# Performance work log

Hardware: AMD Instinct MI355X
Metric: run time of the kernel (lower is better)

## Reference

```python
import jax, jax.numpy as jnp
import numpy as np

GDEP = 2
ALPHA = 0.05

def setup_inputs() -> dict:
    key = jax.random.key(0)
    ks = jax.random.split(key, 6)
    B, C, V, L = 8, 32, 512, 256  # L = c_in * num_patterns
    x = jax.random.normal(ks[0], (B, C, V, L), dtype=jnp.float32)
    adj = jax.random.uniform(ks[1], (B, V, V), dtype=jnp.float32)
    W = jax.random.normal(ks[2], (L, L), dtype=jnp.float32) * (1.0 / np.sqrt(L))
    b = jax.random.normal(ks[3], (L,), dtype=jnp.float32) * (1.0 / np.sqrt(L))
    conv_w = jax.random.normal(ks[4], (C, (GDEP + 1) * C, 1, 1), dtype=jnp.float32) * 0.1
    conv_b = jax.random.normal(ks[5], (C,), dtype=jnp.float32) * 0.1
    return {"x": x, "adj": adj, "W": W, "b": b, "conv_w": conv_w, "conv_b": conv_b}

def reference(x, adj, W, b, conv_w, conv_b):
    B, C, V, L = x.shape
    # adj normalization: add self loops, divide by column-sums (sum over dim 1)
    adj_new = adj + jnp.eye(V, dtype=adj.dtype)[None]          # [B,V,V]
    d = adj_new.sum(axis=1)[:, None, :]                        # [B,1,V]
    a = adj_new / d                                            # [B,V,V]
    h = x
    out = [h]
    for _ in range(GDEP):
        hw = h @ W + b                                         # [B,C,V,L] (matmul on last dim)
        diff = jnp.einsum('ncwl,nvw->ncvl', hw, a)             # hypergraph diffusion over nodes
        h = ALPHA * x + (1.0 - ALPHA) * diff
        out.append(h)
    ho = jnp.concatenate(out, axis=1)                          # [B,(gdep+1)*C,V,L]
    # 1x1 Conv2d == channel-mixing einsum
    w2 = conv_w[:, :, 0, 0]                                    # [C_out, (gdep+1)*C]
    ho = jnp.einsum('bcvl,oc->bovl', ho, w2) + conv_b[None, :, None, None]
    return ho
```

## Files before the change

### kernel.cpp

```cpp
#include <hip/hip_runtime.h>

constexpr int NB = 8;
constexpr int NC = 32;
constexpr int NV = 512;
constexpr int NL = 256;
constexpr float F_ALPHA = 0.05f;
constexpr float F_BETA  = 0.95f;

typedef __bf16 bf16x8 __attribute__((ext_vector_type(8)));
typedef float  f32x4  __attribute__((ext_vector_type(4)));

__device__ __forceinline__ void async_ld16(const void* g, void* l) {
  __builtin_amdgcn_global_load_lds(
      (const __attribute__((address_space(1))) void*)g,
      (__attribute__((address_space(3))) void*)l, 16, 0, 0);
}


__global__ void k_colsum_part(const float* __restrict__ adj, float* __restrict__ partial) {
  int idx = blockIdx.x * 256 + threadIdx.x;
  int w = idx & 511;
  int chunk = (idx >> 9) & 7;
  int n = idx >> 12;
  const float* p = adj + n * (NV * NV) + chunk * 64 * NV + w;
  float s = 0.f;
#pragma unroll
  for (int v = 0; v < 64; ++v) s += p[v * NV];
  partial[idx] = s;
}

__global__ void k_dinv(const float* __restrict__ partial, float* __restrict__ dinv) {
  int idx = blockIdx.x * 256 + threadIdx.x;
  int w = idx & 511;
  int n = idx >> 9;
  float s = 1.f;
#pragma unroll
  for (int j = 0; j < 8; ++j) s += partial[n * 4096 + j * 512 + w];
  dinv[idx] = 1.f / s;
}

__global__ void k_prep_a(const float* __restrict__ adj, const float* __restrict__ dinv,
                         __bf16* __restrict__ a) {
  int idx = blockIdx.x * 256 + threadIdx.x;
  int w = idx & 511;
  int v = (idx >> 9) & 511;
  int n = idx >> 18;
  float val = adj[idx] + (v == w ? 1.0f : 0.0f);
  a[idx] = (__bf16)(val * dinv[(n << 9) | w]);
}

__global__ void k_prep_wt(const float* __restrict__ W, __bf16* __restrict__ Wt) {
  int idx = blockIdx.x * 256 + threadIdx.x;
  int l = idx >> 8, k = idx & 255;
  Wt[idx] = (__bf16)W[(k << 8) | l];
}

__global__ void k_prep_cwt(const float* __restrict__ cw, float* __restrict__ cwT) {
  int idx = blockIdx.x * 256 + threadIdx.x;
  if (idx < 3072) {
    int k = idx >> 5, o = idx & 31;
    cwT[idx] = cw[o * 96 + k];
  }
}

template <bool BF32>
__global__ __launch_bounds__(256, 2)
void k_gemm_wt(const __bf16* __restrict__ Wt, const void* __restrict__ Bsrc,
               const float* __restrict__ bias, __bf16* __restrict__ hw) {
  __shared__ __align__(16) char lds[32768];
  char* ldsA = lds;
  char* ldsB = lds + 16384;

  const int tid = threadIdx.x;
  const int bid = blockIdx.x;
  const int p = bid >> 3;
  const int mtile = (bid >> 2) & 1;
  const int ntile = bid & 3;
  const int n = p >> 5, c = p & 31;

  int Bbase, Bstride;
  if (BF32) { Bbase = p * (NV * NL); Bstride = NL; }
  else      { Bbase = n * (NV * NC * NL) + c * NL; Bstride = NC * NL; }

  const int wave = tid >> 6, lane = tid & 63;
  const int quad = lane >> 4, l16 = lane & 15;
  const int wm = wave >> 1, wn = wave & 1;
  const int wbase = (tid & ~63) * 16;

  f32x4 acc[4][4];
#pragma unroll
  for (int i = 0; i < 4; ++i)
#pragma unroll
    for (int j = 0; j < 4; ++j) acc[i][j] = (f32x4){0.f, 0.f, 0.f, 0.f};

  for (int kt = 0; kt < 256 / 64; ++kt) {
    __syncthreads();
#pragma unroll
    for (int j = 0; j < 4; ++j) {
      int pos = j * 4096 + tid * 16;
      int row = pos >> 7;
      int kb = (pos & 127) ^ ((row & 7) * 16);
      const __bf16* g = Wt + (mtile * 128 + row) * 256 + kt * 64 + (kb >> 1);
      async_ld16(g, ldsA + j * 4096 + wbase);
    }
    if (BF32) {
      const float* Bf = (const float*)Bsrc;
#pragma unroll
      for (int j = 0; j < 4; ++j) {
        int pos = j * 4096 + tid * 16;
        int row = pos >> 7;
        int kb = (pos & 127) ^ ((row & 7) * 16);
        const float* g = Bf + Bbase + (ntile * 128 + row) * Bstride + kt * 64 + (kb >> 1);
        float4 f0 = *(const float4*)g;
        float4 f1 = *(const float4*)(g + 4);
        bf16x8 vv;
        vv[0] = (__bf16)f0.x; vv[1] = (__bf16)f0.y; vv[2] = (__bf16)f0.z; vv[3] = (__bf16)f0.w;
        vv[4] = (__bf16)f1.x; vv[5] = (__bf16)f1.y; vv[6] = (__bf16)f1.z; vv[7] = (__bf16)f1.w;
        *(bf16x8*)(ldsB + pos) = vv;
      }
    } else {
      const __bf16* Bf = (const __bf16*)Bsrc;
#pragma unroll
      for (int j = 0; j < 4; ++j) {
        int pos = j * 4096 + tid * 16;
        int row = pos >> 7;
        int kb = (pos & 127) ^ ((row & 7) * 16);
        const __bf16* g = Bf + Bbase + (ntile * 128 + row) * Bstride + kt * 64 + (kb >> 1);
        async_ld16(g, ldsB + j * 4096 + wbase);
      }
    }
    __syncthreads();
#pragma unroll
    for (int ks = 0; ks < 2; ++ks) {
      bf16x8 af[4], bfr[4];
#pragma unroll
      for (int mb = 0; mb < 4; ++mb) {
        int m = wm * 64 + mb * 16 + l16;
        int kb = (ks * 64 + quad * 16) ^ ((m & 7) * 16);
        af[mb] = *(const bf16x8*)(ldsA + m * 128 + kb);
      }
#pragma unroll
      for (int nb = 0; nb < 4; ++nb) {
        int nn = wn * 64 + nb * 16 + l16;
        int kb = (ks * 64 + quad * 16) ^ ((nn & 7) * 16);
        bfr[nb] = *(const bf16x8*)(ldsB + nn * 128 + kb);
      }
#pragma unroll
      for (int mb = 0; mb < 4; ++mb)
#pragma unroll
        for (int nb = 0; nb < 4; ++nb)
          acc[mb][nb] = __builtin_amdgcn_mfma_f32_16x16x32_bf16(af[mb], bfr[nb], acc[mb][nb], 0, 0, 0);
    }
  }
  __bf16* outp = hw + p * (NL * NV) + mtile * 128 * NV + ntile * 128;
#pragma unroll
  for (int mb = 0; mb < 4; ++mb) {
#pragma unroll
    for (int r = 0; r < 4; ++r) {
      int ml = wm * 64 + mb * 16 + quad * 4 + r;
      float bv = bias[mtile * 128 + ml];
#pragma unroll
      for (int nb = 0; nb < 4; ++nb) {
        int nl = wn * 64 + nb * 16 + l16;
        outp[ml * NV + nl] = (__bf16)(acc[mb][nb][r] + bv);
      }
    }
  }
}

__global__ __launch_bounds__(256, 2)
void k_gemm_a(const __bf16* __restrict__ abuf, const __bf16* __restrict__ hw,
              const float* __restrict__ x, __bf16* __restrict__ hout) {
  __shared__ __align__(16) char lds[32768];
  char* ldsA = lds;
  char* ldsB = lds + 16384;

  const int tid = threadIdx.x;
  const int bid = blockIdx.x;
  const int n = bid >> 8;
  const int mtile = (bid >> 6) & 3;
  const int ntile = bid & 63;

  const __bf16* Ab = abuf + n * (NV * NV) + mtile * 128 * NV;
  const __bf16* Bb = hw + n * (NC * NL * NV) + ntile * 128 * NV;

  const int wave = tid >> 6, lane = tid & 63;
  const int quad = lane >> 4, l16 = lane & 15;
  const int wm = wave >> 1, wn = wave & 1;
  const int wbase = (tid & ~63) * 16;

  f32x4 acc[4][4];
#pragma unroll
  for (int i = 0; i < 4; ++i)
#pragma unroll
    for (int j = 0; j < 4; ++j) acc[i][j] = (f32x4){0.f, 0.f, 0.f, 0.f};

  for (int kt = 0; kt < 512 / 64; ++kt) {
    __syncthreads();
#pragma unroll
    for (int j = 0; j < 4; ++j) {
      int pos = j * 4096 + tid * 16;
      int row = pos >> 7;
      int kb = (pos & 127) ^ ((row & 7) * 16);
      async_ld16(Ab + row * NV + kt * 64 + (kb >> 1), ldsA + j * 4096 + wbase);
    }
#pragma unroll
    for (int j = 0; j < 4; ++j) {
      int pos = j * 4096 + tid * 16;
      int row = pos >> 7;
      int kb = (pos & 127) ^ ((row & 7) * 16);
      async_ld16(Bb + row * NV + kt * 64 + (kb >> 1), ldsB + j * 4096 + wbase);
    }
    __syncthreads();
#pragma unroll
    for (int ks = 0; ks < 2; ++ks) {
      bf16x8 af[4], bfr[4];
#pragma unroll
      for (int mb = 0; mb < 4; ++mb) {
        int m = wm * 64 + mb * 16 + l16;
        int kb = (ks * 64 + quad * 16) ^ ((m & 7) * 16);
        af[mb] = *(const bf16x8*)(ldsA + m * 128 + kb);
      }
#pragma unroll
      for (int nb = 0; nb < 4; ++nb) {
        int nn = wn * 64 + nb * 16 + l16;
        int kb = (ks * 64 + quad * 16) ^ ((nn & 7) * 16);
        bfr[nb] = *(const bf16x8*)(ldsB + nn * 128 + kb);
      }
#pragma unroll
      for (int mb = 0; mb < 4; ++mb)
#pragma unroll
        for (int nb = 0; nb < 4; ++nb)
          acc[mb][nb] = __builtin_amdgcn_mfma_f32_16x16x32_bf16(af[mb], bfr[nb], acc[mb][nb], 0, 0, 0);
    }
  }
#pragma unroll
  for (int mb = 0; mb < 4; ++mb) {
#pragma unroll
    for (int r = 0; r < 4; ++r) {
      int v = mtile * 128 + wm * 64 + mb * 16 + quad * 4 + r;
#pragma unroll
      for (int nb = 0; nb < 4; ++nb) {
        int col = ntile * 128 + wn * 64 + nb * 16 + l16;
        int c = col >> 8, l = col & 255;
        float xv = x[((n * NC + c) * NV + v) * NL + l];
        hout[n * (NV * NC * NL) + v * (NC * NL) + col] =
            (__bf16)(F_ALPHA * xv + F_BETA * acc[mb][nb][r]);
      }
    }
  }
}

__global__ void k_conv_valu(const float* __restrict__ x, const __bf16* __restrict__ h1,
                            const __bf16* __restrict__ h2, const float* __restrict__ cwT,
                            const float* __restrict__ cb, float* __restrict__ out) {
  const int bid = blockIdx.x;
  const int n = bid >> 9, v = bid & 511;
  const int l = threadIdx.x;

  const float*  xp  = x  + n * (NC * NV * NL) + v * NL + l;
  const __bf16* hp1 = h1 + (n * NV + v) * (NC * NL) + l;
  const __bf16* hp2 = h2 + (n * NV + v) * (NC * NL) + l;

  float acc[32];
#pragma unroll
  for (int o = 0; o < 32; ++o) acc[o] = 0.f;

#pragma unroll 2
  for (int c = 0; c < 32; ++c) {
    float xv = xp[c * (NV * NL)];
    float v1 = (float)hp1[c * NL];
    float v2 = (float)hp2[c * NL];
    const float* wx = cwT + c * 32;
    const float* w1 = cwT + (32 + c) * 32;
    const float* w2 = cwT + (64 + c) * 32;
#pragma unroll
    for (int o = 0; o < 32; ++o)
      acc[o] = fmaf(wx[o], xv, fmaf(w1[o], v1, fmaf(w2[o], v2, acc[o])));
  }

  float* op = out + (n * NC * NV + v) * NL + l;
#pragma unroll
  for (int o = 0; o < 32; ++o) op[o * (NV * NL)] = acc[o] + cb[o];
}

extern "C" void kernel_launch(void* const* d_in, const int* in_sizes, int n_in,
                              void* d_out, int out_size, void* d_ws, size_t ws_size,
                              hipStream_t stream) {
  const float* x   = (const float*)d_in[0];
  const float* adj = (const float*)d_in[1];
  const float* W   = (const float*)d_in[2];
  const float* b   = (const float*)d_in[3];
  const float* cw  = (const float*)d_in[4];
  const float* cb  = (const float*)d_in[5];
  float* out = (float*)d_out;
  char* ws = (char*)d_ws;

  float*  dinv    = (float*)ws;
  float*  partial = (float*)(ws + 16384);
  __bf16* Wt      = (__bf16*)(ws + 147456);
  __bf16* abuf    = (__bf16*)(ws + 278528);
  __bf16* hwbuf   = (__bf16*)(ws + 4472832);
  __bf16* h1      = (__bf16*)(ws + 4472832 + 67108864);
  __bf16* h2      = (__bf16*)(ws + 4472832 + 2 * 67108864);
  float*  cwT     = partial;

  k_colsum_part<<<128, 256, 0, stream>>>(adj, partial);
  k_dinv<<<16, 256, 0, stream>>>(partial, dinv);
  k_prep_cwt<<<12, 256, 0, stream>>>(cw, cwT);
  k_prep_a<<<8192, 256, 0, stream>>>(adj, dinv, abuf);
  k_prep_wt<<<256, 256, 0, stream>>>(W, Wt);

  k_gemm_wt<true><<<2048, 256, 0, stream>>>(Wt, (const void*)x, b, hwbuf);
  k_gemm_a<<<2048, 256, 0, stream>>>(abuf, hwbuf, x, h1);
  k_gemm_wt<false><<<2048, 256, 0, stream>>>(Wt, (const void*)h1, b, hwbuf);
  k_gemm_a<<<2048, 256, 0, stream>>>(abuf, hwbuf, x, h2);

  k_conv_valu<<<4096, 256, 0, stream>>>(x, h1, h2, cwT, cb, out);
}
```

Baseline: 508.9 us.

## Fold alpha*x residual into weights to drop fp32 x reads from diffusion epilogues

Uses alpha+beta=1 to rewrite the recurrence so the diffusion GEMM stores only the raw diffusion result D. The second linear GEMM blends in the previous hw buffer as alpha*hwA + beta*(D1 W + b). The 1x1 conv weights are pre-combined so x, D1 and D2 feed the channel mix directly. This removes the strided fp32 x loads from both diffusion GEMM epilogues, at the cost of one extra bf16 read in the second linear GEMM. The conv kernel also gets explicit two-deep software prefetch of its per-channel inputs. Rounding changes slightly because D, rather than h, is now what gets stored in bf16.

```diff
diff --git a/kernel.cpp b/kernel.cpp
--- a/kernel.cpp
+++ b/kernel.cpp
@@ -59,14 +59,18 @@
   int idx = blockIdx.x * 256 + threadIdx.x;
   if (idx < 3072) {
     int k = idx >> 5, o = idx & 31;
-    cwT[idx] = cw[o * 96 + k];
-  }
-}
-
-template <bool BF32>
+    float v;
+    if (k < 32)      v = cw[o * 96 + k] + F_ALPHA * (cw[o * 96 + 32 + k] + cw[o * 96 + 64 + k]);
+    else             v = F_BETA * cw[o * 96 + k];
+    cwT[idx] = v;
+  }
+}
+
+template <bool BF32, int EPI>
 __global__ __launch_bounds__(256, 2)
 void k_gemm_wt(const __bf16* __restrict__ Wt, const void* __restrict__ Bsrc,
-               const float* __restrict__ bias, __bf16* __restrict__ hw) {
+               const float* __restrict__ bias, __bf16* __restrict__ hw,
+               const __bf16* __restrict__ hwprev) {
   __shared__ __align__(16) char lds[32768];
   char* ldsA = lds;
   char* ldsB = lds + 16384;
@@ -152,7 +156,9 @@
           acc[mb][nb] = __builtin_amdgcn_mfma_f32_16x16x32_bf16(af[mb], bfr[nb], acc[mb][nb], 0, 0, 0);
     }
   }
-  __bf16* outp = hw + p * (NL * NV) + mtile * 128 * NV + ntile * 128;
+  const size_t obase = (size_t)p * (NL * NV) + mtile * 128 * NV + ntile * 128;
+  __bf16* outp = hw + obase;
+  const __bf16* prevp = (EPI == 1) ? hwprev + obase : nullptr;
 #pragma unroll
   for (int mb = 0; mb < 4; ++mb) {
 #pragma unroll
@@ -162,7 +168,12 @@
 #pragma unroll
       for (int nb = 0; nb < 4; ++nb) {
         int nl = wn * 64 + nb * 16 + l16;
-        outp[ml * NV + nl] = (__bf16)(acc[mb][nb][r] + bv);
+        if (EPI == 0) {
+          outp[ml * NV + nl] = (__bf16)(acc[mb][nb][r] + bv);
+        } else {
+          float pv = (float)prevp[ml * NV + nl];
+          outp[ml * NV + nl] = (__bf16)(F_ALPHA * pv + F_BETA * (acc[mb][nb][r] + bv));
+        }
       }
     }
   }
@@ -170,7 +181,7 @@
 
 __global__ __launch_bounds__(256, 2)
 void k_gemm_a(const __bf16* __restrict__ abuf, const __bf16* __restrict__ hw,
-              const float* __restrict__ x, __bf16* __restrict__ hout) {
+              __bf16* __restrict__ dout) {
   __shared__ __align__(16) char lds[32768];
   char* ldsA = lds;
   char* ldsB = lds + 16384;
@@ -242,35 +253,43 @@
 #pragma unroll
       for (int nb = 0; nb < 4; ++nb) {
         int col = ntile * 128 + wn * 64 + nb * 16 + l16;
-        int c = col >> 8, l = col & 255;
-        float xv = x[((n * NC + c) * NV + v) * NL + l];
-        hout[n * (NV * NC * NL) + v * (NC * NL) + col] =
-            (__bf16)(F_ALPHA * xv + F_BETA * acc[mb][nb][r]);
-      }
-    }
-  }
-}
-
-__global__ void k_conv_valu(const float* __restrict__ x, const __bf16* __restrict__ h1,
-                            const __bf16* __restrict__ h2, const float* __restrict__ cwT,
+        dout[n * (NV * NC * NL) + v * (NC * NL) + col] = (__bf16)acc[mb][nb][r];
+      }
+    }
+  }
+}
+
+__global__ void k_conv_valu(const float* __restrict__ x, const __bf16* __restrict__ d1,
+                            const __bf16* __restrict__ d2, const float* __restrict__ cwT,
                             const float* __restrict__ cb, float* __restrict__ out) {
   const int bid = blockIdx.x;
   const int n = bid >> 9, v = bid & 511;
   const int l = threadIdx.x;
 
-  const float*  xp  = x  + n * (NC * NV * NL) + v * NL + l;
-  const __bf16* hp1 = h1 + (n * NV + v) * (NC * NL) + l;
-  const __bf16* hp2 = h2 + (n * NV + v) * (NC * NL) + l;
+  const float*  xp = x  + n * (NC * NV * NL) + v * NL + l;
+  const __bf16* p1 = d1 + (n * NV + v) * (NC * NL) + l;
+  const __bf16* p2 = d2 + (n * NV + v) * (NC * NL) + l;
 
   float acc[32];
 #pragma unroll
   for (int o = 0; o < 32; ++o) acc[o] = 0.f;
 
-#pragma unroll 2
+  float  xs[2];
+  __bf16 a1[2], a2[2];
+  xs[0] = xp[0];            a1[0] = p1[0];   a2[0] = p2[0];
+  xs[1] = xp[NV * NL];      a1[1] = p1[NL];  a2[1] = p2[NL];
+
+#pragma unroll
   for (int c = 0; c < 32; ++c) {
-    float xv = xp[c * (NV * NL)];
-    float v1 = (float)hp1[c * NL];
-    float v2 = (float)hp2[c * NL];
+    const int slot = c & 1;
+    float xv = xs[slot];
+    float v1 = (float)a1[slot];
+    float v2 = (float)a2[slot];
+    if (c + 2 < 32) {
+      xs[slot] = xp[(c + 2) * (NV * NL)];
+      a1[slot] = p1[(c + 2) * NL];
+      a2[slot] = p2[(c + 2) * NL];
+    }
     const float* wx = cwT + c * 32;
     const float* w1 = cwT + (32 + c) * 32;
     const float* w2 = cwT + (64 + c) * 32;
@@ -300,10 +319,15 @@
   float*  partial = (float*)(ws + 16384);
   __bf16* Wt      = (__bf16*)(ws + 147456);
   __bf16* abuf    = (__bf16*)(ws + 278528);
-  __bf16* hwbuf   = (__bf16*)(ws + 4472832);
-  __bf16* h1      = (__bf16*)(ws + 4472832 + 67108864);
-  __bf16* h2      = (__bf16*)(ws + 4472832 + 2 * 67108864);
+  __bf16* slot1   = (__bf16*)(ws + 4472832);
+  __bf16* slot2   = (__bf16*)(ws + 4472832 + 67108864);
+  __bf16* slot3   = (__bf16*)(ws + 4472832 + 2 * 67108864);
   float*  cwT     = partial;
+
+  __bf16* hwA = slot1;
+  __bf16* D1  = slot2;
+  __bf16* hwB = slot3;
+  __bf16* D2  = slot1;
 
   k_colsum_part<<<128, 256, 0, stream>>>(adj, partial);
   k_dinv<<<16, 256, 0, stream>>>(partial, dinv);
@@ -311,10 +335,9 @@
   k_prep_a<<<8192, 256, 0, stream>>>(adj, dinv, abuf);
   k_prep_wt<<<256, 256, 0, stream>>>(W, Wt);
 
-  k_gemm_wt<true><<<2048, 256, 0, stream>>>(Wt, (const void*)x, b, hwbuf);
-  k_gemm_a<<<2048, 256, 0, stream>>>(abuf, hwbuf, x, h1);
-  k_gemm_wt<false><<<2048, 256, 0, stream>>>(Wt, (const void*)h1, b, hwbuf);
-  k_gemm_a<<<2048, 256, 0, stream>>>(abuf, hwbuf, x, h2);
-
-  k_conv_valu<<<4096, 256, 0, stream>>>(x, h1, h2, cwT, cb, out);
-}
+  k_gemm_wt<true, 0><<<2048, 256, 0, stream>>>(Wt, (const void*)x, b, hwA, nullptr);
+  k_gemm_a<<<2048, 256, 0, stream>>>(abuf, hwA, D1);
+  k_gemm_wt<false, 1><<<2048, 256, 0, stream>>>(Wt, (const void*)D1, b, hwB, hwA);
+  k_gemm_a<<<2048, 256, 0, stream>>>(abuf, hwB, D2);
+  k_conv_valu<<<4096, 256, 0, stream>>>(x, D1, D2, cwT, cb, out);
+}
```

After: 512.2 us. About the same (+0.7%).
